# Optimization experiments

Hardware: AMD Instinct MI355X
Metric: run time of the kernel (lower is better)

The kernel has to match this reference:

```python
import jax, jax.numpy as jnp
import numpy as np

# Model constants (match init_kwargs / torchcde conventions)
B = 1024        # batch
L = 128         # number of spline knots (grid_points = 0..L-1)
C_IN = 8        # input_channels
HID = 64        # hidden_channels
MLP_H = 128     # CDEFunc hidden width
INIT_H = 20     # initial-network hidden width


def setup_inputs() -> dict:
    key = jax.random.key(0)
    ks = jax.random.split(key, 9)
    # cubic spline coeffs: (B, L-1, 4*C_IN) laid out as [a, b, c, d] per interval
    coeffs = jax.random.normal(ks[0], (B, L - 1, 4 * C_IN), dtype=jnp.float32) * 0.1
    # initial network: C_IN -> 20 -> HID (ReLU, then Tanh)
    Wi1 = jax.random.normal(ks[1], (C_IN, INIT_H), dtype=jnp.float32) / np.sqrt(C_IN)
    bi1 = jnp.zeros((INIT_H,), jnp.float32)
    Wi2 = jax.random.normal(ks[2], (INIT_H, HID), dtype=jnp.float32) / np.sqrt(INIT_H)
    bi2 = jnp.zeros((HID,), jnp.float32)
    # CDE vector field: (HID+1) -> 128 -> C_IN*HID (ReLU, then Tanh)
    W1 = jax.random.normal(ks[3], (HID + 1, MLP_H), dtype=jnp.float32) / np.sqrt(HID + 1)
    b1 = jnp.zeros((MLP_H,), jnp.float32)
    W2 = jax.random.normal(ks[4], (MLP_H, C_IN * HID), dtype=jnp.float32) / np.sqrt(MLP_H)
    b2 = jnp.zeros((C_IN * HID,), jnp.float32)
    return {"coeffs": coeffs, "Wi1": Wi1, "bi1": bi1, "Wi2": Wi2, "bi2": bi2,
            "W1": W1, "b1": b1, "W2": W2, "b2": b2}


def reference(coeffs, Wi1, bi1, Wi2, bi2, W1, b1, W2, b2):
    Lm1 = coeffs.shape[1]
    # a,b,c,d: each (B, L-1, C_IN). X(t) = a + b*f + c*f^2 + d*f^3 on interval idx,
    # dX/dt = b + 2c*f + 3d*f^2, with f = t - idx (torchcde CubicSpline convention).
    a, b, c, d = jnp.split(coeffs, 4, axis=-1)

    def dXdt(t):
        idx = jnp.clip(jnp.floor(t).astype(jnp.int32), 0, Lm1 - 1)
        fr = t - idx
        return b[:, idx] + 2.0 * c[:, idx] * fr + 3.0 * d[:, idx] * fr * fr  # (B, C_IN)

    def cde_func(t, z):
        # FFN([HID+1, 128, C_IN*HID], ReLU hidden, Tanh output) on concat(t, z)
        tz = jnp.concatenate([jnp.full((z.shape[0], 1), t, z.dtype), z], axis=1)
        h = jax.nn.relu(tz @ W1 + b1)
        return jnp.tanh(h @ W2 + b2).reshape(z.shape[0], HID, C_IN)  # (B, HID, C_IN)

    def vf(t, z):
        # dz/dt = f(t,z) @ dX/dt
        return jnp.einsum('bhc,bc->bh', cde_func(t, z), dXdt(t))

    # z0 = initial(X(t0)); X(0) = a at interval 0 with frac 0
    X0 = a[:, 0]
    z0 = jnp.tanh(jax.nn.relu(X0 @ Wi1 + bi1) @ Wi2 + bi2)  # (B, HID)

    def rk4_step(z, i):
        t = i.astype(z.dtype)
        k1 = vf(t, z)
        k2 = vf(t + 0.5, z + 0.5 * k1)
        k3 = vf(t + 0.5, z + 0.5 * k2)
        k4 = vf(t + 1.0, z + k3)
        z_new = z + (k1 + 2.0 * k2 + 2.0 * k3 + k4) / 6.0
        return z_new, z_new

    _, zs = jax.lax.scan(rk4_step, z0, jnp.arange(Lm1))  # (L-1, B, HID)
    # z evaluated at all grid points, like cdeint(t=X.grid_points): (B, L, HID)
    return jnp.concatenate([z0[None], zs], axis=0).transpose(1, 0, 2)
```

## Files before the change

kernel.cpp:

```cpp
#include <hip/hip_runtime.h>
#include <stdint.h>

#define LM1  127
#define NTHR 512

typedef _Float16 half8_t __attribute__((ext_vector_type(8)));
typedef float    f32x4   __attribute__((ext_vector_type(4)));

__device__ __forceinline__ float fast_tanh(float x) {
  float e = __expf(2.0f * x);
  return 1.0f - 2.0f * __builtin_amdgcn_rcpf(e + 1.0f);
}

#define BAR() asm volatile("s_waitcnt lgkmcnt(0)\n\ts_barrier" ::: "memory")

__global__ void __launch_bounds__(NTHR, 2) cde_kernel(
    const float* __restrict__ coeffs,
    const float* __restrict__ Wi1, const float* __restrict__ bi1,
    const float* __restrict__ Wi2, const float* __restrict__ bi2,
    const float* __restrict__ W1,  const float* __restrict__ b1,
    const float* __restrict__ W2,  const float* __restrict__ b2,
    float* __restrict__ out)
{
  __shared__ __align__(16) _Float16 zsb[1024];
  __shared__ __align__(16) _Float16 hA [2048];
  __shared__ __align__(16) float    fwb[8][288];
  __shared__ __align__(16) float    gds[2][3][4][8];

  const int t    = threadIdx.x;
  const int lane = t & 63;
  const int w    = t >> 6;
  const int l15  = lane & 15;
  const int lq   = lane >> 4;
  const int row0 = blockIdx.x * 4;

  for (int u = t; u < 512;  u += NTHR) ((uint32_t*)zsb)[u] = 0u;
  for (int u = t; u < 1024; u += NTHR) ((uint32_t*)hA)[u]  = 0u;

  half8_t bB[2];
  #pragma unroll
  for (int kt = 0; kt < 2; ++kt)
    #pragma unroll
    for (int j = 0; j < 8; ++j)
      bB[kt][j] = (_Float16)W1[(1 + kt * 32 + lq * 8 + j) * 128 + w * 16 + l15];
  const float w1t_c = W1[w * 16 + l15];
  const float b1_c  = b1[w * 16 + l15];
  _Float16* hwp;
  {
    const int col = 16 * w + l15;
    const int ktw = (col >> 5) & 3, lqw2 = (col >> 3) & 3, j2 = col & 7;
    hwp = &hA[8 * (ktw * 64 + lqw2 * 16) + j2];
  }

  half8_t bf[4][4];
  #pragma unroll
  for (int nt = 0; nt < 4; ++nt)
    #pragma unroll
    for (int kt = 0; kt < 4; ++kt)
      #pragma unroll
      for (int j = 0; j < 8; ++j)
        bf[nt][kt][j] =
            (_Float16)W2[(kt * 32 + lq * 8 + j) * 512 + w * 64 + nt * 16 + l15];

  const int r_ = lane & 3;
  const int hh = (lane >> 2) & 7;
  const int cp = lane >> 5;
  const float* bp = b2 + w * 64 + hh * 8 + cp * 4;
  const float b2c0 = bp[0], b2c1 = bp[1], b2c2 = bp[2], b2c3 = bp[3];
  const int frbase = 36 * hh + 16 * cp + r_;
  const int hx = 8 * w + hh;

  _Float16* zwp;
  {
    const int kh = hx >> 5, lqw = (hx >> 3) & 3, jj = hx & 7;
    zwp = &zsb[8 * (kh * 64 + lqw * 16 + r_) + jj];
  }
  float* const fsp = &fwb[w][36 * (l15 >> 3) + 4 * (l15 & 7)];

  float z = 0.0f;
  if (lane < 32) {
    const float* cb = coeffs + (size_t)(row0 + r_) * (LM1 * 32);
    float x0[8];
    #pragma unroll
    for (int c = 0; c < 8; ++c) x0[c] = cb[c];
    float acc = bi2[hx];
    for (int j = 0; j < 20; ++j) {
      float u = bi1[j];
      #pragma unroll
      for (int c = 0; c < 8; ++c) u += x0[c] * Wi1[c * 20 + j];
      acc += fmaxf(u, 0.0f) * Wi2[j * 64 + hx];
    }
    z = fast_tanh(acc);
    out[(size_t)(row0 + r_) * 8192 + hx] = z;
  }

  const int rg = (lane >> 3) & 3, cg = lane & 7;
  const float* cbp = coeffs + (size_t)(row0 + rg) * (LM1 * 32);
  float pb = 0.f, pc = 0.f, pd = 0.f, pbn = 0.f;
  const bool stg = (w == 7) && (lane < 32);
  if (stg) { pb = cbp[8 + cg]; pc = cbp[16 + cg]; pd = cbp[24 + cg]; pbn = cbp[40 + cg]; }

  __syncthreads();

  for (int i = 0; i < LM1; ++i) {
    if (stg) {
      gds[i & 1][0][rg][cg] = pb;
      gds[i & 1][1][rg][cg] = pb + pc + 0.75f * pd;
      gds[i & 1][2][rg][cg] = (i < LM1 - 1) ? pbn : fmaf(3.0f, pd, fmaf(2.0f, pc, pb));
      if (i + 1 < LM1) {
        const float* nb = cbp + (size_t)(i + 1) * 32;
        pb = nb[8 + cg]; pc = nb[16 + cg]; pd = nb[24 + cg];
        pbn = (i + 2 < LM1) ? nb[40 + cg] : 0.0f;
      }
    }

    float ksum = 0.0f, kprev = 0.0f;
    #pragma unroll
    for (int s = 0; s < 4; ++s) {
      const float coef = (s == 0) ? 0.0f : (s == 3) ? 1.0f : 0.5f;
      const float ts   = (float)i + ((s == 0) ? 0.0f : (s == 3) ? 1.0f : 0.5f);
      const int   gi   = (s == 0) ? 0 : (s == 3) ? 2 : 1;

      if (lane < 32) *zwp = (_Float16)(z + coef * kprev);
      BAR();

      {
        const half8_t a0 = *(const half8_t*)(zsb + 8 * lane);
        const half8_t a1 = *(const half8_t*)(zsb + 512 + 8 * lane);
        f32x4 hd = {0.f, 0.f, 0.f, 0.f};
        hd = __builtin_amdgcn_mfma_f32_16x16x32_f16(a0, bB[0], hd, 0, 0, 0);
        hd = __builtin_amdgcn_mfma_f32_16x16x32_f16(a1, bB[1], hd, 0, 0, 0);
        if (lane < 16) {
          const float hb = fmaf(ts, w1t_c, b1_c);
          hwp[0]  = (_Float16)fmaxf(hd.x + hb, 0.0f);
          hwp[8]  = (_Float16)fmaxf(hd.y + hb, 0.0f);
          hwp[16] = (_Float16)fmaxf(hd.z + hb, 0.0f);
          hwp[24] = (_Float16)fmaxf(hd.w + hb, 0.0f);
        }
      }
      BAR();

      {
        const f32x4 gv = *(const f32x4*)&gds[i & 1][gi][r_][4 * cp];

        half8_t ha[4];
        #pragma unroll
        for (int kt = 0; kt < 4; ++kt)
          ha[kt] = *(const half8_t*)(hA + 512 * kt + 8 * lane);
        f32x4 d0 = {0.f, 0.f, 0.f, 0.f}, d1 = d0, d2 = d0, d3 = d0;
        #pragma unroll
        for (int kt = 0; kt < 4; ++kt) {
          d0 = __builtin_amdgcn_mfma_f32_16x16x32_f16(ha[kt], bf[0][kt], d0, 0, 0, 0);
          d1 = __builtin_amdgcn_mfma_f32_16x16x32_f16(ha[kt], bf[1][kt], d1, 0, 0, 0);
          d2 = __builtin_amdgcn_mfma_f32_16x16x32_f16(ha[kt], bf[2][kt], d2, 0, 0, 0);
          d3 = __builtin_amdgcn_mfma_f32_16x16x32_f16(ha[kt], bf[3][kt], d3, 0, 0, 0);
        }
        if (lane < 16) {
          *(f32x4*)(fsp)       = d0;
          *(f32x4*)(fsp + 72)  = d1;
          *(f32x4*)(fsp + 144) = d2;
          *(f32x4*)(fsp + 216) = d3;
        }
        asm volatile("s_waitcnt lgkmcnt(0)" ::: "memory");

        const float* fb = &fwb[w][frbase];
        const float v0 = fb[0], v1 = fb[4], v2 = fb[8], v3 = fb[12];
        float kcv = fast_tanh(v0 + b2c0) * gv.x + fast_tanh(v1 + b2c1) * gv.y
                  + fast_tanh(v2 + b2c2) * gv.z + fast_tanh(v3 + b2c3) * gv.w;
        {
          int a = __float_as_int(kcv), b = a;
          asm volatile("v_permlane32_swap_b32 %0, %1" : "+v"(a), "+v"(b));
          kcv = __int_as_float(a) + __int_as_float(b);
        }
        kprev = kcv;
        ksum += ((s == 1 || s == 2) ? 2.0f : 1.0f) * kcv;
      }
    }
    if (lane < 32) {
      z += ksum * (1.0f / 6.0f);
      out[(size_t)(row0 + r_) * 8192 + (size_t)(i + 1) * 64 + hx] = z;
    }
  }
}

extern "C" void kernel_launch(void* const* d_in, const int* in_sizes, int n_in,
                              void* d_out, int out_size, void* d_ws, size_t ws_size,
                              hipStream_t stream) {
  const float* coeffs = (const float*)d_in[0];
  const float* Wi1    = (const float*)d_in[1];
  const float* bi1    = (const float*)d_in[2];
  const float* Wi2    = (const float*)d_in[3];
  const float* bi2    = (const float*)d_in[4];
  const float* W1     = (const float*)d_in[5];
  const float* b1     = (const float*)d_in[6];
  const float* W2     = (const float*)d_in[7];
  const float* b2     = (const float*)d_in[8];
  float* out          = (float*)d_out;
  (void)in_sizes; (void)n_in; (void)out_size; (void)d_ws; (void)ws_size;
  cde_kernel<<<256, NTHR, 0, stream>>>(coeffs, Wi1, bi1, Wi2, bi2,
                                       W1, b1, W2, b2, out);
}
```

Measured before the change: 537.9 us.

## Compute first MLP layer redundantly per wave to drop one barrier per RK stage

Each wave now computes the full 128-wide hidden layer itself, with W1 staged in LDS, and writes it into a private per-wave hA buffer. This removes the block-wide barrier between the two MLP layers. The z state and time-bias vectors are double-buffered so that a single barrier per RK stage is enough, and the coefficient staging is moved to the end of the step. The cost is 8x redundant first-layer MFMA work, more LDS traffic and a larger LDS footprint, which may hurt occupancy at 2 blocks per CU.

After: 879.6 us. 63.5% more time.

```diff
diff --git a/kernel.cpp b/kernel.cpp
--- a/kernel.cpp
+++ b/kernel.cpp
@@ -5,7 +5,9 @@
 #define NTHR 512
 
 typedef _Float16 half8_t __attribute__((ext_vector_type(8)));
+typedef _Float16 half4_t __attribute__((ext_vector_type(4)));
 typedef float    f32x4   __attribute__((ext_vector_type(4)));
+typedef float    f32x2   __attribute__((ext_vector_type(2)));
 
 __device__ __forceinline__ float fast_tanh(float x) {
   float e = __expf(2.0f * x);
@@ -22,10 +24,12 @@
     const float* __restrict__ W2,  const float* __restrict__ b2,
     float* __restrict__ out)
 {
-  __shared__ __align__(16) _Float16 zsb[1024];
-  __shared__ __align__(16) _Float16 hA [2048];
+  __shared__ __align__(16) _Float16 wlds[8192];
+  __shared__ __align__(16) _Float16 zsbT[2][1024];
+  __shared__ __align__(16) _Float16 hA[8][2048];
   __shared__ __align__(16) float    fwb[8][288];
   __shared__ __align__(16) float    gds[2][3][4][8];
+  __shared__ __align__(16) float    ubuf[2][128];
 
   const int t    = threadIdx.x;
   const int lane = t & 63;
@@ -34,23 +38,14 @@
   const int lq   = lane >> 4;
   const int row0 = blockIdx.x * 4;
 
-  for (int u = t; u < 512;  u += NTHR) ((uint32_t*)zsb)[u] = 0u;
-  for (int u = t; u < 1024; u += NTHR) ((uint32_t*)hA)[u]  = 0u;
-
-  half8_t bB[2];
-  #pragma unroll
-  for (int kt = 0; kt < 2; ++kt)
-    #pragma unroll
-    for (int j = 0; j < 8; ++j)
-      bB[kt][j] = (_Float16)W1[(1 + kt * 32 + lq * 8 + j) * 128 + w * 16 + l15];
-  const float w1t_c = W1[w * 16 + l15];
-  const float b1_c  = b1[w * 16 + l15];
-  _Float16* hwp;
-  {
-    const int col = 16 * w + l15;
-    const int ktw = (col >> 5) & 3, lqw2 = (col >> 3) & 3, j2 = col & 7;
-    hwp = &hA[8 * (ktw * 64 + lqw2 * 16) + j2];
-  }
+  for (int u = t; u < 1024; u += NTHR) ((uint32_t*)zsbT)[u] = 0u;
+
+  for (int idx = t; idx < 8192; idx += NTHR) {
+    const int m = idx >> 10, kt = (idx >> 9) & 1, L = (idx >> 3) & 63, j = idx & 7;
+    wlds[idx] = (_Float16)W1[(1 + 8 * (L >> 4) + j + 32 * kt) * 128 + 16 * m + (L & 15)];
+  }
+
+  __syncthreads();
 
   half8_t bf[4][4];
   #pragma unroll
@@ -61,6 +56,14 @@
       for (int j = 0; j < 8; ++j)
         bf[nt][kt][j] =
             (_Float16)W2[(kt * 32 + lq * 8 + j) * 512 + w * 64 + nt * 16 + l15];
+
+  float w10a = 0.f, w10b = 0.f, b1a = 0.f, b1b = 0.f;
+  if (w == 0) {
+    w10a = W1[2 * lane]; w10b = W1[2 * lane + 1];
+    b1a  = b1[2 * lane]; b1b  = b1[2 * lane + 1];
+    f32x2 u0 = {b1a, b1b};
+    *(f32x2*)&ubuf[0][2 * lane] = u0;
+  }
 
   const int r_ = lane & 3;
   const int hh = (lane >> 2) & 7;
@@ -69,13 +72,11 @@
   const float b2c0 = bp[0], b2c1 = bp[1], b2c2 = bp[2], b2c3 = bp[3];
   const int frbase = 36 * hh + 16 * cp + r_;
   const int hx = 8 * w + hh;
-
-  _Float16* zwp;
-  {
-    const int kh = hx >> 5, lqw = (hx >> 3) & 3, jj = hx & 7;
-    zwp = &zsb[8 * (kh * 64 + lqw * 16 + r_) + jj];
-  }
+  const int zoff = 8 * r_ + 128 * ((hx >> 3) & 3) + 512 * (hx >> 5) + (hx & 7);
   float* const fsp = &fwb[w][36 * (l15 >> 3) + 4 * (l15 & 7)];
+
+  _Float16* const hAw = &hA[w][0];
+  const int hbase = 8 * l15 + 4 * (lq & 1) + 128 * (lq >> 1);
 
   float z = 0.0f;
   if (lane < 32) {
@@ -91,94 +92,114 @@
       acc += fmaxf(u, 0.0f) * Wi2[j * 64 + hx];
     }
     z = fast_tanh(acc);
+    zsbT[0][zoff] = (_Float16)z;
     out[(size_t)(row0 + r_) * 8192 + hx] = z;
   }
 
   const int rg = (lane >> 3) & 3, cg = lane & 7;
   const float* cbp = coeffs + (size_t)(row0 + rg) * (LM1 * 32);
-  float pb = 0.f, pc = 0.f, pd = 0.f, pbn = 0.f;
   const bool stg = (w == 7) && (lane < 32);
-  if (stg) { pb = cbp[8 + cg]; pc = cbp[16 + cg]; pd = cbp[24 + cg]; pbn = cbp[40 + cg]; }
+  float pb2 = 0.f, pc2 = 0.f, pd2 = 0.f, pbn2 = 0.f;
+  if (stg) {
+    const float pb = cbp[8 + cg], pc = cbp[16 + cg], pd = cbp[24 + cg], pbn = cbp[40 + cg];
+    gds[0][0][rg][cg] = pb;
+    gds[0][1][rg][cg] = pb + pc + 0.75f * pd;
+    gds[0][2][rg][cg] = pbn;
+  }
 
   __syncthreads();
 
   for (int i = 0; i < LM1; ++i) {
-    if (stg) {
-      gds[i & 1][0][rg][cg] = pb;
-      gds[i & 1][1][rg][cg] = pb + pc + 0.75f * pd;
-      gds[i & 1][2][rg][cg] = (i < LM1 - 1) ? pbn : fmaf(3.0f, pd, fmaf(2.0f, pc, pb));
-      if (i + 1 < LM1) {
-        const float* nb = cbp + (size_t)(i + 1) * 32;
-        pb = nb[8 + cg]; pc = nb[16 + cg]; pd = nb[24 + cg];
-        pbn = (i + 2 < LM1) ? nb[40 + cg] : 0.0f;
-      }
+    if (stg && i + 1 < LM1) {
+      const float* nb = cbp + (size_t)(i + 1) * 32;
+      pb2 = nb[8 + cg]; pc2 = nb[16 + cg]; pd2 = nb[24 + cg];
+      pbn2 = (i + 2 < LM1) ? nb[40 + cg] : 0.0f;
     }
 
-    float ksum = 0.0f, kprev = 0.0f;
+    float ksum = 0.0f;
     #pragma unroll
     for (int s = 0; s < 4; ++s) {
-      const float coef = (s == 0) ? 0.0f : (s == 3) ? 1.0f : 0.5f;
-      const float ts   = (float)i + ((s == 0) ? 0.0f : (s == 3) ? 1.0f : 0.5f);
-      const int   gi   = (s == 0) ? 0 : (s == 3) ? 2 : 1;
-
-      if (lane < 32) *zwp = (_Float16)(z + coef * kprev);
+      const int rb   = s & 1;
+      const int wbuf = rb ^ 1;
+      const int gi   = (s == 0) ? 0 : (s == 3) ? 2 : 1;
+      const float tnext = (float)i + ((s < 2) ? 0.5f : 1.0f);
+
+      const half8_t zb0 = *(const half8_t*)(&zsbT[rb][8 * lane]);
+      const half8_t zb1 = *(const half8_t*)(&zsbT[rb][8 * lane + 512]);
+      const f32x4 gv = *(const f32x4*)&gds[i & 1][gi][r_][4 * cp];
+
+      #pragma unroll
+      for (int m = 0; m < 8; ++m) {
+        const half8_t af0 = *(const half8_t*)(&wlds[(2 * m    ) * 512 + 8 * lane]);
+        const half8_t af1 = *(const half8_t*)(&wlds[(2 * m + 1) * 512 + 8 * lane]);
+        f32x4 acc = {0.f, 0.f, 0.f, 0.f};
+        acc = __builtin_amdgcn_mfma_f32_16x16x32_f16(af0, zb0, acc, 0, 0, 0);
+        acc = __builtin_amdgcn_mfma_f32_16x16x32_f16(af1, zb1, acc, 0, 0, 0);
+        const f32x4 uv = *(const f32x4*)&ubuf[rb][16 * m + 4 * lq];
+        half4_t hv;
+        hv[0] = (_Float16)fmaxf(acc.x + uv.x, 0.0f);
+        hv[1] = (_Float16)fmaxf(acc.y + uv.y, 0.0f);
+        hv[2] = (_Float16)fmaxf(acc.z + uv.z, 0.0f);
+        hv[3] = (_Float16)fmaxf(acc.w + uv.w, 0.0f);
+        *(half4_t*)(hAw + hbase + 256 * m) = hv;
+      }
+      asm volatile("s_waitcnt lgkmcnt(0)" ::: "memory");
+
+      half8_t ha[4];
+      #pragma unroll
+      for (int kt = 0; kt < 4; ++kt)
+        ha[kt] = *(const half8_t*)(hAw + 8 * lane + 512 * kt);
+      f32x4 d0 = {0.f, 0.f, 0.f, 0.f}, d1 = d0, d2 = d0, d3 = d0;
+      #pragma unroll
+      for (int kt = 0; kt < 4; ++kt) {
+        d0 = __builtin_amdgcn_mfma_f32_16x16x32_f16(ha[kt], bf[0][kt], d0, 0, 0, 0);
+        d1 = __builtin_amdgcn_mfma_f32_16x16x32_f16(ha[kt], bf[1][kt], d1, 0, 0, 0);
+        d2 = __builtin_amdgcn_mfma_f32_16x16x32_f16(ha[kt], bf[2][kt], d2, 0, 0, 0);
+        d3 = __builtin_amdgcn_mfma_f32_16x16x32_f16(ha[kt], bf[3][kt], d3, 0, 0, 0);
+      }
+      if (lane < 16) {
+        *(f32x4*)(fsp)       = d0;
+        *(f32x4*)(fsp + 72)  = d1;
+        *(f32x4*)(fsp + 144) = d2;
+        *(f32x4*)(fsp + 216) = d3;
+      }
+      asm volatile("s_waitcnt lgkmcnt(0)" ::: "memory");
+
+      const float* fb = &fwb[w][frbase];
+      const float v0 = fb[0], v1 = fb[4], v2 = fb[8], v3 = fb[12];
+      float kcv = fast_tanh(v0 + b2c0) * gv.x + fast_tanh(v1 + b2c1) * gv.y
+                + fast_tanh(v2 + b2c2) * gv.z + fast_tanh(v3 + b2c3) * gv.w;
+      {
+        int a = __float_as_int(kcv), b;
+        asm volatile("v_mov_b32 %1, %0\n\t"
+                     "v_permlane32_swap_b32 %0, %1"
+                     : "+v"(a), "=&v"(b));
+        kcv = __int_as_float(a) + __int_as_float(b);
+      }
+      ksum += ((s == 1 || s == 2) ? 2.0f : 1.0f) * kcv;
+
+      if (w == 0) {
+        f32x2 un = {fmaf(tnext, w10a, b1a), fmaf(tnext, w10b, b1b)};
+        *(f32x2*)&ubuf[wbuf][2 * lane] = un;
+      }
+      if (s < 3) {
+        const float cn = (s == 2) ? 1.0f : 0.5f;
+        if (lane < 32) zsbT[wbuf][zoff] = (_Float16)(z + cn * kcv);
+      } else {
+        if (lane < 32) {
+          z = fmaf(ksum, 1.0f / 6.0f, z);
+          zsbT[wbuf][zoff] = (_Float16)z;
+          out[(size_t)(row0 + r_) * 8192 + (size_t)(i + 1) * 64 + hx] = z;
+        }
+        if (stg && i + 1 < LM1) {
+          const int ii = i + 1;
+          gds[ii & 1][0][rg][cg] = pb2;
+          gds[ii & 1][1][rg][cg] = pb2 + pc2 + 0.75f * pd2;
+          gds[ii & 1][2][rg][cg] =
+              (ii < LM1 - 1) ? pbn2 : fmaf(3.0f, pd2, fmaf(2.0f, pc2, pb2));
+        }
+      }
       BAR();
-
-      {
-        const half8_t a0 = *(const half8_t*)(zsb + 8 * lane);
-        const half8_t a1 = *(const half8_t*)(zsb + 512 + 8 * lane);
-        f32x4 hd = {0.f, 0.f, 0.f, 0.f};
-        hd = __builtin_amdgcn_mfma_f32_16x16x32_f16(a0, bB[0], hd, 0, 0, 0);
-        hd = __builtin_amdgcn_mfma_f32_16x16x32_f16(a1, bB[1], hd, 0, 0, 0);
-        if (lane < 16) {
-          const float hb = fmaf(ts, w1t_c, b1_c);
-          hwp[0]  = (_Float16)fmaxf(hd.x + hb, 0.0f);
-          hwp[8]  = (_Float16)fmaxf(hd.y + hb, 0.0f);
-          hwp[16] = (_Float16)fmaxf(hd.z + hb, 0.0f);
-          hwp[24] = (_Float16)fmaxf(hd.w + hb, 0.0f);
-        }
-      }
-      BAR();
-
-      {
-        const f32x4 gv = *(const f32x4*)&gds[i & 1][gi][r_][4 * cp];
-
-        half8_t ha[4];
-        #pragma unroll
-        for (int kt = 0; kt < 4; ++kt)
-          ha[kt] = *(const half8_t*)(hA + 512 * kt + 8 * lane);
-        f32x4 d0 = {0.f, 0.f, 0.f, 0.f}, d1 = d0, d2 = d0, d3 = d0;
-        #pragma unroll
-        for (int kt = 0; kt < 4; ++kt) {
-          d0 = __builtin_amdgcn_mfma_f32_16x16x32_f16(ha[kt], bf[0][kt], d0, 0, 0, 0);
-          d1 = __builtin_amdgcn_mfma_f32_16x16x32_f16(ha[kt], bf[1][kt], d1, 0, 0, 0);
-          d2 = __builtin_amdgcn_mfma_f32_16x16x32_f16(ha[kt], bf[2][kt], d2, 0, 0, 0);
-          d3 = __builtin_amdgcn_mfma_f32_16x16x32_f16(ha[kt], bf[3][kt], d3, 0, 0, 0);
-        }
-        if (lane < 16) {
-          *(f32x4*)(fsp)       = d0;
-          *(f32x4*)(fsp + 72)  = d1;
-          *(f32x4*)(fsp + 144) = d2;
-          *(f32x4*)(fsp + 216) = d3;
-        }
-        asm volatile("s_waitcnt lgkmcnt(0)" ::: "memory");
-
-        const float* fb = &fwb[w][frbase];
-        const float v0 = fb[0], v1 = fb[4], v2 = fb[8], v3 = fb[12];
-        float kcv = fast_tanh(v0 + b2c0) * gv.x + fast_tanh(v1 + b2c1) * gv.y
-                  + fast_tanh(v2 + b2c2) * gv.z + fast_tanh(v3 + b2c3) * gv.w;
-        {
-          int a = __float_as_int(kcv), b = a;
-          asm volatile("v_permlane32_swap_b32 %0, %1" : "+v"(a), "+v"(b));
-          kcv = __int_as_float(a) + __int_as_float(b);
-        }
-        kprev = kcv;
-        ksum += ((s == 1 || s == 2) ? 2.0f : 1.0f) * kcv;
-      }
-    }
-    if (lane < 32) {
-      z += ksum * (1.0f / 6.0f);
-      out[(size_t)(row0 + r_) * 8192 + (size_t)(i + 1) * 64 + hx] = z;
     }
   }
 }
```

## Halve block to 4 waves, each wave computing double the MLP columns

Applied to the files above, without the earlier changes.

Cuts the block from 8 to 4 wavefronts. Each wave now owns 32 hidden units in the first layer and 128 output columns in the second layer. W2 fragments held in registers double, and each lane reduces all 8 channels itself, so the permlane swap goes away. Fewer waves means cheaper barriers per RK4 stage and all lanes doing useful epilogue work, at the cost of more serial MFMA work per wave, higher register pressure, and one block per CU instead of two.

After: 603.6 us. 12.2% more time.

```diff
diff --git a/kernel.cpp b/kernel.cpp
--- a/kernel.cpp
+++ b/kernel.cpp
@@ -2,7 +2,7 @@
 #include <stdint.h>
 
 #define LM1  127
-#define NTHR 512
+#define NTHR 256
 
 typedef _Float16 half8_t __attribute__((ext_vector_type(8)));
 typedef float    f32x4   __attribute__((ext_vector_type(4)));
@@ -14,7 +14,7 @@
 
 #define BAR() asm volatile("s_waitcnt lgkmcnt(0)\n\ts_barrier" ::: "memory")
 
-__global__ void __launch_bounds__(NTHR, 2) cde_kernel(
+__global__ void __launch_bounds__(NTHR, 1) cde_kernel(
     const float* __restrict__ coeffs,
     const float* __restrict__ Wi1, const float* __restrict__ bi1,
     const float* __restrict__ Wi2, const float* __restrict__ bi2,
@@ -24,7 +24,7 @@
 {
   __shared__ __align__(16) _Float16 zsb[1024];
   __shared__ __align__(16) _Float16 hA [2048];
-  __shared__ __align__(16) float    fwb[8][288];
+  __shared__ __align__(16) float    fwb[4][544];
   __shared__ __align__(16) float    gds[2][3][4][8];
 
   const int t    = threadIdx.x;
@@ -37,48 +37,54 @@
   for (int u = t; u < 512;  u += NTHR) ((uint32_t*)zsb)[u] = 0u;
   for (int u = t; u < 1024; u += NTHR) ((uint32_t*)hA)[u]  = 0u;
 
-  half8_t bB[2];
+  half8_t bB[2][2];
+  float w1t_c[2], b1_c[2];
   #pragma unroll
-  for (int kt = 0; kt < 2; ++kt)
-    #pragma unroll
-    for (int j = 0; j < 8; ++j)
-      bB[kt][j] = (_Float16)W1[(1 + kt * 32 + lq * 8 + j) * 128 + w * 16 + l15];
-  const float w1t_c = W1[w * 16 + l15];
-  const float b1_c  = b1[w * 16 + l15];
-  _Float16* hwp;
-  {
-    const int col = 16 * w + l15;
+  for (int nt = 0; nt < 2; ++nt) {
+    #pragma unroll
+    for (int kt = 0; kt < 2; ++kt)
+      #pragma unroll
+      for (int j = 0; j < 8; ++j)
+        bB[nt][kt][j] =
+            (_Float16)W1[(1 + kt * 32 + lq * 8 + j) * 128 + 32 * w + 16 * nt + l15];
+    w1t_c[nt] = W1[32 * w + 16 * nt + l15];
+    b1_c[nt]  = b1[32 * w + 16 * nt + l15];
+  }
+  _Float16* hwp[2];
+  #pragma unroll
+  for (int nt = 0; nt < 2; ++nt) {
+    const int col = 32 * w + 16 * nt + l15;
     const int ktw = (col >> 5) & 3, lqw2 = (col >> 3) & 3, j2 = col & 7;
-    hwp = &hA[8 * (ktw * 64 + lqw2 * 16) + j2];
-  }
-
-  half8_t bf[4][4];
+    hwp[nt] = &hA[8 * (ktw * 64 + lqw2 * 16) + j2];
+  }
+
+  half8_t bf[8][4];
   #pragma unroll
-  for (int nt = 0; nt < 4; ++nt)
+  for (int nt = 0; nt < 8; ++nt)
     #pragma unroll
     for (int kt = 0; kt < 4; ++kt)
       #pragma unroll
       for (int j = 0; j < 8; ++j)
         bf[nt][kt][j] =
-            (_Float16)W2[(kt * 32 + lq * 8 + j) * 512 + w * 64 + nt * 16 + l15];
+            (_Float16)W2[(kt * 32 + lq * 8 + j) * 512 + 128 * w + nt * 16 + l15];
 
   const int r_ = lane & 3;
-  const int hh = (lane >> 2) & 7;
-  const int cp = lane >> 5;
-  const float* bp = b2 + w * 64 + hh * 8 + cp * 4;
-  const float b2c0 = bp[0], b2c1 = bp[1], b2c2 = bp[2], b2c3 = bp[3];
-  const int frbase = 36 * hh + 16 * cp + r_;
-  const int hx = 8 * w + hh;
+  const int hh = lane >> 2;
+  const int hx = 16 * w + hh;
+  const float* b2p = b2 + 8 * hx;
+  const f32x4 b2lo = *(const f32x4*)b2p;
+  const f32x4 b2hi = *(const f32x4*)(b2p + 4);
 
   _Float16* zwp;
   {
     const int kh = hx >> 5, lqw = (hx >> 3) & 3, jj = hx & 7;
     zwp = &zsb[8 * (kh * 64 + lqw * 16 + r_) + jj];
   }
-  float* const fsp = &fwb[w][36 * (l15 >> 3) + 4 * (l15 & 7)];
-
-  float z = 0.0f;
-  if (lane < 32) {
+  float* const fsp = &fwb[w][4 * l15];
+  const float* const frp = &fwb[w][68 * (hh >> 1) + 32 * (hh & 1) + r_];
+
+  float z;
+  {
     const float* cb = coeffs + (size_t)(row0 + r_) * (LM1 * 32);
     float x0[8];
     #pragma unroll
@@ -97,7 +103,7 @@
   const int rg = (lane >> 3) & 3, cg = lane & 7;
   const float* cbp = coeffs + (size_t)(row0 + rg) * (LM1 * 32);
   float pb = 0.f, pc = 0.f, pd = 0.f, pbn = 0.f;
-  const bool stg = (w == 7) && (lane < 32);
+  const bool stg = (w == 3) && (lane < 32);
   if (stg) { pb = cbp[8 + cg]; pc = cbp[16 + cg]; pd = cbp[24 + cg]; pbn = cbp[40 + cg]; }
 
   __syncthreads();
@@ -121,65 +127,70 @@
       const float ts   = (float)i + ((s == 0) ? 0.0f : (s == 3) ? 1.0f : 0.5f);
       const int   gi   = (s == 0) ? 0 : (s == 3) ? 2 : 1;
 
-      if (lane < 32) *zwp = (_Float16)(z + coef * kprev);
+      *zwp = (_Float16)(z + coef * kprev);
       BAR();
 
       {
         const half8_t a0 = *(const half8_t*)(zsb + 8 * lane);
         const half8_t a1 = *(const half8_t*)(zsb + 512 + 8 * lane);
-        f32x4 hd = {0.f, 0.f, 0.f, 0.f};
-        hd = __builtin_amdgcn_mfma_f32_16x16x32_f16(a0, bB[0], hd, 0, 0, 0);
-        hd = __builtin_amdgcn_mfma_f32_16x16x32_f16(a1, bB[1], hd, 0, 0, 0);
+        f32x4 hd[2];
+        #pragma unroll
+        for (int nt = 0; nt < 2; ++nt) {
+          f32x4 acc = {0.f, 0.f, 0.f, 0.f};
+          acc = __builtin_amdgcn_mfma_f32_16x16x32_f16(a0, bB[nt][0], acc, 0, 0, 0);
+          acc = __builtin_amdgcn_mfma_f32_16x16x32_f16(a1, bB[nt][1], acc, 0, 0, 0);
+          hd[nt] = acc;
+        }
         if (lane < 16) {
-          const float hb = fmaf(ts, w1t_c, b1_c);
-          hwp[0]  = (_Float16)fmaxf(hd.x + hb, 0.0f);
-          hwp[8]  = (_Float16)fmaxf(hd.y + hb, 0.0f);
-          hwp[16] = (_Float16)fmaxf(hd.z + hb, 0.0f);
-          hwp[24] = (_Float16)fmaxf(hd.w + hb, 0.0f);
+          #pragma unroll
+          for (int nt = 0; nt < 2; ++nt) {
+            const float hb = fmaf(ts, w1t_c[nt], b1_c[nt]);
+            hwp[nt][0]  = (_Float16)fmaxf(hd[nt].x + hb, 0.0f);
+            hwp[nt][8]  = (_Float16)fmaxf(hd[nt].y + hb, 0.0f);
+            hwp[nt][16] = (_Float16)fmaxf(hd[nt].z + hb, 0.0f);
+            hwp[nt][24] = (_Float16)fmaxf(hd[nt].w + hb, 0.0f);
+          }
         }
       }
       BAR();
 
       {
-        const f32x4 gv = *(const f32x4*)&gds[i & 1][gi][r_][4 * cp];
+        const f32x4 gva = *(const f32x4*)&gds[i & 1][gi][r_][0];
+        const f32x4 gvb = *(const f32x4*)&gds[i & 1][gi][r_][4];
 
         half8_t ha[4];
         #pragma unroll
         for (int kt = 0; kt < 4; ++kt)
-          ha[kt] = *(const half8_t*)(hA + 512 * kt + 8 * lane);
-        f32x4 d0 = {0.f, 0.f, 0.f, 0.f}, d1 = d0, d2 = d0, d3 = d0;
-        #pragma unroll
-        for (int kt = 0; kt < 4; ++kt) {
-          d0 = __builtin_amdgcn_mfma_f32_16x16x32_f16(ha[kt], bf[0][kt], d0, 0, 0, 0);
-          d1 = __builtin_amdgcn_mfma_f32_16x16x32_f16(ha[kt], bf[1][kt], d1, 0, 0, 0);
-          d2 = __builtin_amdgcn_mfma_f32_16x16x32_f16(ha[kt], bf[2][kt], d2, 0, 0, 0);
-          d3 = __builtin_amdgcn_mfma_f32_16x16x32_f16(ha[kt], bf[3][kt], d3, 0, 0, 0);
-        }
+          ha[kt] = *(const half8_t*)(hA + 8 * lane + 512 * kt);
+        f32x4 d[8];
+        #pragma unroll
+        for (int nt = 0; nt < 8; ++nt) d[nt] = (f32x4){0.f, 0.f, 0.f, 0.f};
+        #pragma unroll
+        for (int kt = 0; kt < 4; ++kt)
+          #pragma unroll
+          for (int nt = 0; nt < 8; ++nt)
+            d[nt] = __builtin_amdgcn_mfma_f32_16x16x32_f16(ha[kt], bf[nt][kt], d[nt], 0, 0, 0);
         if (lane < 16) {
-          *(f32x4*)(fsp)       = d0;
-          *(f32x4*)(fsp + 72)  = d1;
-          *(f32x4*)(fsp + 144) = d2;
-          *(f32x4*)(fsp + 216) = d3;
+          #pragma unroll
+          for (int nt = 0; nt < 8; ++nt)
+            *(f32x4*)(fsp + 68 * nt) = d[nt];
         }
         asm volatile("s_waitcnt lgkmcnt(0)" ::: "memory");
 
-        const float* fb = &fwb[w][frbase];
-        const float v0 = fb[0], v1 = fb[4], v2 = fb[8], v3 = fb[12];
-        float kcv = fast_tanh(v0 + b2c0) * gv.x + fast_tanh(v1 + b2c1) * gv.y
-                  + fast_tanh(v2 + b2c2) * gv.z + fast_tanh(v3 + b2c3) * gv.w;
-        {
-          int a = __float_as_int(kcv), b = a;
-          asm volatile("v_permlane32_swap_b32 %0, %1" : "+v"(a), "+v"(b));
-          kcv = __int_as_float(a) + __int_as_float(b);
-        }
+        float kcv = fast_tanh(frp[0]  + b2lo.x) * gva.x
+                  + fast_tanh(frp[4]  + b2lo.y) * gva.y
+                  + fast_tanh(frp[8]  + b2lo.z) * gva.z
+                  + fast_tanh(frp[12] + b2lo.w) * gva.w
+                  + fast_tanh(frp[16] + b2hi.x) * gvb.x
+                  + fast_tanh(frp[20] + b2hi.y) * gvb.y
+                  + fast_tanh(frp[24] + b2hi.z) * gvb.z
+                  + fast_tanh(frp[28] + b2hi.w) * gvb.w;
         kprev = kcv;
         ksum += ((s == 1 || s == 2) ? 2.0f : 1.0f) * kcv;
       }
     }
-    if (lane < 32) {
-      z += ksum * (1.0f / 6.0f);
-      out[(size_t)(row0 + r_) * 8192 + (size_t)(i + 1) * 64 + hx] = z;
-    }
+    z += ksum * (1.0f / 6.0f);
+    out[(size_t)(row0 + r_) * 8192 + (size_t)(i + 1) * 64 + hx] = z;
   }
 }
 
```

## Transpose MFMA operands so outputs land in registers, removing LDS round-trip

Applied to the files above, without the earlier changes.

Swaps the A/B operands of both MFMA stages so that weights are the A operand and activations the B operand. Each lane then holds output rows whose layout matches the tanh/dX contraction directly. This removes the fwb scratch buffer, its LDS store/waitcnt/reload, and the permlane swap, which is replaced by a shuffle. It also double-buffers the z staging buffer, so there is one barrier fewer per RK stage. In exchange, the tanh work is replicated across lanes where only a few rows are valid, and register pressure from the extra state rises.

After: 605.0 us. 12.5% more time.

```diff
diff --git a/kernel.cpp b/kernel.cpp
--- a/kernel.cpp
+++ b/kernel.cpp
@@ -5,6 +5,7 @@
 #define NTHR 512
 
 typedef _Float16 half8_t __attribute__((ext_vector_type(8)));
+typedef _Float16 half4_t __attribute__((ext_vector_type(4)));
 typedef float    f32x4   __attribute__((ext_vector_type(4)));
 
 __device__ __forceinline__ float fast_tanh(float x) {
@@ -22,9 +23,8 @@
     const float* __restrict__ W2,  const float* __restrict__ b2,
     float* __restrict__ out)
 {
-  __shared__ __align__(16) _Float16 zsb[1024];
-  __shared__ __align__(16) _Float16 hA [2048];
-  __shared__ __align__(16) float    fwb[8][288];
+  __shared__ __align__(16) _Float16 zsbT[2][1024];
+  __shared__ __align__(16) _Float16 hA[2048];
   __shared__ __align__(16) float    gds[2][3][4][8];
 
   const int t    = threadIdx.x;
@@ -32,66 +32,75 @@
   const int w    = t >> 6;
   const int l15  = lane & 15;
   const int lq   = lane >> 4;
+  const int lqh  = lq >> 1, lql = lq & 1;
+  const int r4   = l15 & 3;
+  const bool rowok = (l15 < 4);
   const int row0 = blockIdx.x * 4;
 
-  for (int u = t; u < 512;  u += NTHR) ((uint32_t*)zsb)[u] = 0u;
-  for (int u = t; u < 1024; u += NTHR) ((uint32_t*)hA)[u]  = 0u;
-
-  half8_t bB[2];
+  for (int u = t; u < 1024; u += NTHR) ((uint32_t*)zsbT)[u] = 0u;
+
+  half8_t wA[2];
   #pragma unroll
   for (int kt = 0; kt < 2; ++kt)
     #pragma unroll
     for (int j = 0; j < 8; ++j)
-      bB[kt][j] = (_Float16)W1[(1 + kt * 32 + lq * 8 + j) * 128 + w * 16 + l15];
-  const float w1t_c = W1[w * 16 + l15];
-  const float b1_c  = b1[w * 16 + l15];
-  _Float16* hwp;
+      wA[kt][j] = (_Float16)W1[(1 + 32 * kt + 8 * lq + j) * 128 + 16 * w + l15];
+
+  f32x4 w1t4, b14;
+  #pragma unroll
+  for (int reg = 0; reg < 4; ++reg) {
+    w1t4[reg] = W1[16 * w + 4 * lq + reg];
+    b14[reg]  = b1[16 * w + 4 * lq + reg];
+  }
+
+  half8_t wf[4][4];
+  #pragma unroll
+  for (int mt = 0; mt < 4; ++mt)
+    #pragma unroll
+    for (int kt = 0; kt < 4; ++kt)
+      #pragma unroll
+      for (int j = 0; j < 8; ++j)
+        wf[mt][kt][j] =
+            (_Float16)W2[(32 * kt + 8 * lq + j) * 512 + 64 * w + 16 * mt + l15];
+
+  f32x4 b2v[4];
+  #pragma unroll
+  for (int mt = 0; mt < 4; ++mt)
+    b2v[mt] = *(const f32x4*)&b2[64 * w + 16 * mt + 4 * lq];
+
+  _Float16* const hwp = &hA[128 * (2 * w + lqh) + 8 * l15 + 4 * lql];
+  const int zbase = 128 * w + 8 * l15;
+  const int dA = 4 * lql + lqh;
+  const int dB = 4 * lql + 2 + lqh;
+
+  float z[4];
   {
-    const int col = 16 * w + l15;
-    const int ktw = (col >> 5) & 3, lqw2 = (col >> 3) & 3, j2 = col & 7;
-    hwp = &hA[8 * (ktw * 64 + lqw2 * 16) + j2];
-  }
-
-  half8_t bf[4][4];
-  #pragma unroll
-  for (int nt = 0; nt < 4; ++nt)
-    #pragma unroll
-    for (int kt = 0; kt < 4; ++kt)
-      #pragma unroll
-      for (int j = 0; j < 8; ++j)
-        bf[nt][kt][j] =
-            (_Float16)W2[(kt * 32 + lq * 8 + j) * 512 + w * 64 + nt * 16 + l15];
-
-  const int r_ = lane & 3;
-  const int hh = (lane >> 2) & 7;
-  const int cp = lane >> 5;
-  const float* bp = b2 + w * 64 + hh * 8 + cp * 4;
-  const float b2c0 = bp[0], b2c1 = bp[1], b2c2 = bp[2], b2c3 = bp[3];
-  const int frbase = 36 * hh + 16 * cp + r_;
-  const int hx = 8 * w + hh;
-
-  _Float16* zwp;
-  {
-    const int kh = hx >> 5, lqw = (hx >> 3) & 3, jj = hx & 7;
-    zwp = &zsb[8 * (kh * 64 + lqw * 16 + r_) + jj];
-  }
-  float* const fsp = &fwb[w][36 * (l15 >> 3) + 4 * (l15 & 7)];
-
-  float z = 0.0f;
-  if (lane < 32) {
-    const float* cb = coeffs + (size_t)(row0 + r_) * (LM1 * 32);
+    const float* cb = coeffs + (size_t)(row0 + r4) * (LM1 * 32);
     float x0[8];
     #pragma unroll
     for (int c = 0; c < 8; ++c) x0[c] = cb[c];
-    float acc = bi2[hx];
+    float acc[4];
+    #pragma unroll
+    for (int mt = 0; mt < 4; ++mt) acc[mt] = bi2[8 * w + 2 * mt + lqh];
     for (int j = 0; j < 20; ++j) {
-      float u = bi1[j];
-      #pragma unroll
-      for (int c = 0; c < 8; ++c) u += x0[c] * Wi1[c * 20 + j];
-      acc += fmaxf(u, 0.0f) * Wi2[j * 64 + hx];
+      float uj = bi1[j];
+      #pragma unroll
+      for (int c = 0; c < 8; ++c) uj += x0[c] * Wi1[c * 20 + j];
+      uj = fmaxf(uj, 0.0f);
+      #pragma unroll
+      for (int mt = 0; mt < 4; ++mt) acc[mt] += uj * Wi2[j * 64 + 8 * w + 2 * mt + lqh];
     }
-    z = fast_tanh(acc);
-    out[(size_t)(row0 + r_) * 8192 + hx] = z;
+    #pragma unroll
+    for (int mt = 0; mt < 4; ++mt) z[mt] = fast_tanh(acc[mt]);
+  }
+  if (rowok) {
+    const float zA = lql ? z[2] : z[0];
+    const float zB = lql ? z[3] : z[1];
+    zsbT[0][zbase + dA] = (_Float16)zA;
+    zsbT[0][zbase + dB] = (_Float16)zB;
+    float* op = out + (size_t)(row0 + l15) * 8192 + 8 * w;
+    op[dA] = zA;
+    op[dB] = zB;
   }
 
   const int rg = (lane >> 3) & 3, cg = lane & 7;
@@ -114,71 +123,81 @@
       }
     }
 
-    float ksum = 0.0f, kprev = 0.0f;
+    float ksum[4] = {0.f, 0.f, 0.f, 0.f};
     #pragma unroll
     for (int s = 0; s < 4; ++s) {
-      const float coef = (s == 0) ? 0.0f : (s == 3) ? 1.0f : 0.5f;
-      const float ts   = (float)i + ((s == 0) ? 0.0f : (s == 3) ? 1.0f : 0.5f);
-      const int   gi   = (s == 0) ? 0 : (s == 3) ? 2 : 1;
-
-      if (lane < 32) *zwp = (_Float16)(z + coef * kprev);
+      const int   rb = s & 1, wb = rb ^ 1;
+      const int   gi = (s == 0) ? 0 : (s == 3) ? 2 : 1;
+      const float ts = (float)i + ((s == 0) ? 0.0f : (s == 3) ? 1.0f : 0.5f);
+
+      const half8_t zb0 = *(const half8_t*)(&zsbT[rb][8 * lane]);
+      const half8_t zb1 = *(const half8_t*)(&zsbT[rb][512 + 8 * lane]);
+      f32x4 hd = {0.f, 0.f, 0.f, 0.f};
+      hd = __builtin_amdgcn_mfma_f32_16x16x32_f16(wA[0], zb0, hd, 0, 0, 0);
+      hd = __builtin_amdgcn_mfma_f32_16x16x32_f16(wA[1], zb1, hd, 0, 0, 0);
+      half4_t hv;
+      hv[0] = (_Float16)fmaxf(hd.x + fmaf(ts, w1t4.x, b14.x), 0.0f);
+      hv[1] = (_Float16)fmaxf(hd.y + fmaf(ts, w1t4.y, b14.y), 0.0f);
+      hv[2] = (_Float16)fmaxf(hd.z + fmaf(ts, w1t4.z, b14.z), 0.0f);
+      hv[3] = (_Float16)fmaxf(hd.w + fmaf(ts, w1t4.w, b14.w), 0.0f);
+      *(half4_t*)hwp = hv;
       BAR();
 
-      {
-        const half8_t a0 = *(const half8_t*)(zsb + 8 * lane);
-        const half8_t a1 = *(const half8_t*)(zsb + 512 + 8 * lane);
-        f32x4 hd = {0.f, 0.f, 0.f, 0.f};
-        hd = __builtin_amdgcn_mfma_f32_16x16x32_f16(a0, bB[0], hd, 0, 0, 0);
-        hd = __builtin_amdgcn_mfma_f32_16x16x32_f16(a1, bB[1], hd, 0, 0, 0);
-        if (lane < 16) {
-          const float hb = fmaf(ts, w1t_c, b1_c);
-          hwp[0]  = (_Float16)fmaxf(hd.x + hb, 0.0f);
-          hwp[8]  = (_Float16)fmaxf(hd.y + hb, 0.0f);
-          hwp[16] = (_Float16)fmaxf(hd.z + hb, 0.0f);
-          hwp[24] = (_Float16)fmaxf(hd.w + hb, 0.0f);
+      const f32x4 gv = *(const f32x4*)&gds[i & 1][gi][r4][4 * lql];
+      half8_t hb[4];
+      #pragma unroll
+      for (int kt = 0; kt < 4; ++kt)
+        hb[kt] = *(const half8_t*)(&hA[512 * kt + 8 * lane]);
+      f32x4 d0 = {0.f, 0.f, 0.f, 0.f}, d1 = d0, d2 = d0, d3 = d0;
+      #pragma unroll
+      for (int kt = 0; kt < 4; ++kt) {
+        d0 = __builtin_amdgcn_mfma_f32_16x16x32_f16(wf[0][kt], hb[kt], d0, 0, 0, 0);
+        d1 = __builtin_amdgcn_mfma_f32_16x16x32_f16(wf[1][kt], hb[kt], d1, 0, 0, 0);
+        d2 = __builtin_amdgcn_mfma_f32_16x16x32_f16(wf[2][kt], hb[kt], d2, 0, 0, 0);
+        d3 = __builtin_amdgcn_mfma_f32_16x16x32_f16(wf[3][kt], hb[kt], d3, 0, 0, 0);
+      }
+      const float p0 = fast_tanh(d0.x + b2v[0].x) * gv.x + fast_tanh(d0.y + b2v[0].y) * gv.y
+                     + fast_tanh(d0.z + b2v[0].z) * gv.z + fast_tanh(d0.w + b2v[0].w) * gv.w;
+      const float p1 = fast_tanh(d1.x + b2v[1].x) * gv.x + fast_tanh(d1.y + b2v[1].y) * gv.y
+                     + fast_tanh(d1.z + b2v[1].z) * gv.z + fast_tanh(d1.w + b2v[1].w) * gv.w;
+      const float p2 = fast_tanh(d2.x + b2v[2].x) * gv.x + fast_tanh(d2.y + b2v[2].y) * gv.y
+                     + fast_tanh(d2.z + b2v[2].z) * gv.z + fast_tanh(d2.w + b2v[2].w) * gv.w;
+      const float p3 = fast_tanh(d3.x + b2v[3].x) * gv.x + fast_tanh(d3.y + b2v[3].y) * gv.y
+                     + fast_tanh(d3.z + b2v[3].z) * gv.z + fast_tanh(d3.w + b2v[3].w) * gv.w;
+      const float kcv0 = p0 + __shfl_xor(p0, 16, 64);
+      const float kcv1 = p1 + __shfl_xor(p1, 16, 64);
+      const float kcv2 = p2 + __shfl_xor(p2, 16, 64);
+      const float kcv3 = p3 + __shfl_xor(p3, 16, 64);
+      const float wgt = (s == 1 || s == 2) ? 2.0f : 1.0f;
+      ksum[0] += wgt * kcv0;
+      ksum[1] += wgt * kcv1;
+      ksum[2] += wgt * kcv2;
+      ksum[3] += wgt * kcv3;
+
+      if (s < 3) {
+        const float cn = (s == 2) ? 1.0f : 0.5f;
+        if (rowok) {
+          const float zA = lql ? z[2] : z[0], kA = lql ? kcv2 : kcv0;
+          const float zB = lql ? z[3] : z[1], kB = lql ? kcv3 : kcv1;
+          zsbT[wb][zbase + dA] = (_Float16)fmaf(cn, kA, zA);
+          zsbT[wb][zbase + dB] = (_Float16)fmaf(cn, kB, zB);
+        }
+      } else {
+        z[0] = fmaf(ksum[0], 1.0f / 6.0f, z[0]);
+        z[1] = fmaf(ksum[1], 1.0f / 6.0f, z[1]);
+        z[2] = fmaf(ksum[2], 1.0f / 6.0f, z[2]);
+        z[3] = fmaf(ksum[3], 1.0f / 6.0f, z[3]);
+        if (rowok) {
+          const float zA = lql ? z[2] : z[0];
+          const float zB = lql ? z[3] : z[1];
+          zsbT[wb][zbase + dA] = (_Float16)zA;
+          zsbT[wb][zbase + dB] = (_Float16)zB;
+          float* op = out + (size_t)(row0 + l15) * 8192 + (size_t)(i + 1) * 64 + 8 * w;
+          op[dA] = zA;
+          op[dB] = zB;
         }
       }
       BAR();
-
-      {
-        const f32x4 gv = *(const f32x4*)&gds[i & 1][gi][r_][4 * cp];
-
-        half8_t ha[4];
-        #pragma unroll
-        for (int kt = 0; kt < 4; ++kt)
-          ha[kt] = *(const half8_t*)(hA + 512 * kt + 8 * lane);
-        f32x4 d0 = {0.f, 0.f, 0.f, 0.f}, d1 = d0, d2 = d0, d3 = d0;
-        #pragma unroll
-        for (int kt = 0; kt < 4; ++kt) {
-          d0 = __builtin_amdgcn_mfma_f32_16x16x32_f16(ha[kt], bf[0][kt], d0, 0, 0, 0);
-          d1 = __builtin_amdgcn_mfma_f32_16x16x32_f16(ha[kt], bf[1][kt], d1, 0, 0, 0);
-          d2 = __builtin_amdgcn_mfma_f32_16x16x32_f16(ha[kt], bf[2][kt], d2, 0, 0, 0);
-          d3 = __builtin_amdgcn_mfma_f32_16x16x32_f16(ha[kt], bf[3][kt], d3, 0, 0, 0);
-        }
-        if (lane < 16) {
-          *(f32x4*)(fsp)       = d0;
-          *(f32x4*)(fsp + 72)  = d1;
-          *(f32x4*)(fsp + 144) = d2;
-          *(f32x4*)(fsp + 216) = d3;
-        }
-        asm volatile("s_waitcnt lgkmcnt(0)" ::: "memory");
-
-        const float* fb = &fwb[w][frbase];
-        const float v0 = fb[0], v1 = fb[4], v2 = fb[8], v3 = fb[12];
-        float kcv = fast_tanh(v0 + b2c0) * gv.x + fast_tanh(v1 + b2c1) * gv.y
-                  + fast_tanh(v2 + b2c2) * gv.z + fast_tanh(v3 + b2c3) * gv.w;
-        {
-          int a = __float_as_int(kcv), b = a;
-          asm volatile("v_permlane32_swap_b32 %0, %1" : "+v"(a), "+v"(b));
-          kcv = __int_as_float(a) + __int_as_float(b);
-        }
-        kprev = kcv;
-        ksum += ((s == 1 || s == 2) ? 2.0f : 1.0f) * kcv;
-      }
-    }
-    if (lane < 32) {
-      z += ksum * (1.0f / 6.0f);
-      out[(size_t)(row0 + r_) * 8192 + (size_t)(i + 1) * 64 + hx] = z;
     }
   }
 }
```
